# Optimization experiments

Hardware: AMD Instinct MI355X
Metric: run time of the kernel (lower is better)

Reference implementation:

```python
import jax, jax.numpy as jnp
import numpy as np

N_USER, N_ITEM, D = 100000, 50000, 64
H, S, B, L, SUPP, E, HID = 4, 500, 1024, 50, 10000, 1500000, 64

def setup_inputs() -> dict:
    key = jax.random.key(0)
    ks = jax.random.split(key, 24)
    f = lambda k, shp: (jax.random.normal(k, shp, jnp.float32) * 0.1)
    inp = {
        'x': jax.random.randint(ks[0], (B, 2), 0, 50000),
        'history': jax.random.randint(ks[1], (B, L), 0, N_ITEM),
        'history_len': jax.random.randint(ks[2], (B,), 1, L + 1),
        'sample_index': jax.random.randint(ks[3], (H, B, S), 0, SUPP),
        'supp_users': jax.random.randint(ks[4], (SUPP,), 0, N_USER),
        'edge_index': jax.random.randint(ks[5], (2, E), 0, 50000),
        'user_embedding': f(ks[6], (N_USER, D)),
        'item_embedding': f(ks[7], (N_ITEM, D)),
        'wq': f(ks[8], (H, D, D)),
        'wk': f(ks[9], (H, D, D)),
        'wv': f(ks[10], (H, D, D)),
        'w_out_w': f(ks[11], (H * D, D)),
        'gcn_user_w': f(ks[12], (D, D)), 'gcn_user_b': jnp.full((D,), 0.1, jnp.float32),
        'gcn_item_w': f(ks[13], (D, D)), 'gcn_item_b': jnp.full((D,), 0.1, jnp.float32),
        'l1_w': f(ks[14], (4 * D, 2 * HID)), 'l1_b': jnp.full((2 * HID,), 0.1, jnp.float32),
        'l2_w': f(ks[15], (2 * HID, HID)), 'l2_b': jnp.full((HID,), 0.1, jnp.float32),
        'l3_w': f(ks[16], (HID, 1)), 'l3_b': jnp.full((1,), 0.1, jnp.float32),
        'user_bias': jnp.zeros((N_USER, 1), jnp.float32),
        'item_bias': jnp.zeros((N_ITEM, 1), jnp.float32),
    }
    return inp


def _forward(x, history, history_len, sample_index, supp_users, edge_index,
             user_embedding, item_embedding, wq, wk, wv, w_out_w,
             gcn_user_w, gcn_user_b, gcn_item_w, gcn_item_b,
             l1_w, l1_b, l2_w, l2_b, l3_w, l3_b, user_bias, item_bias):
    user_id = x[:, 0]
    item_id = x[:, 1]
    # user init embedding: mean of history item embeddings (original sums unmasked, divides by len)
    user_init_emb = jnp.sum(item_embedding[history], axis=1) / history_len[:, None].astype(jnp.float32)  # [B,D]

    # multi-head RelationGAT over randomly sampled support users
    samp_emb = user_embedding[supp_users[sample_index]]            # [H,B,S,D]
    q = jnp.einsum('bd,hde->hbe', user_init_emb, wq)               # [H,B,D]
    k = jnp.einsum('hbsd,hde->hbse', samp_emb, wk)                 # [H,B,S,D]
    attn = jax.nn.softmax(jnp.einsum('hbe,hbse->hbs', q, k), axis=-1)
    ctx = jnp.einsum('hbs,hbse->hbe', attn, k)                     # [H,B,D]
    gat = jnp.einsum('hbe,hef->hbf', ctx, wv)                      # [H,B,D]
    gat = jnp.transpose(gat, (1, 0, 2)).reshape(gat.shape[1], -1)  # [B,H*D]
    user_emb = gat @ w_out_w                                       # [B,D]

    item_emb = item_embedding[item_id]

    # sparse GCN aggregation via segment_sum (eval mode: no edge dropout)
    eu, ei = edge_index[0], edge_index[1]
    ones_e = jnp.ones((eu.shape[0],), jnp.float32)
    agg_item = jax.ops.segment_sum(item_embedding[ei], eu, num_segments=N_USER)[user_id]
    agg_user = jax.ops.segment_sum(user_embedding[eu], ei, num_segments=N_ITEM)[item_id]
    deg_u = jax.ops.segment_sum(ones_e, eu, num_segments=N_USER)[user_id][:, None] + 1.0
    deg_i = jax.ops.segment_sum(ones_e, ei, num_segments=N_ITEM)[item_id][:, None] + 1.0
    gcn_item_h = agg_item / deg_u
    gcn_user_h = agg_user / deg_i
    gcn_user_out = jax.nn.relu(gcn_user_h @ gcn_user_w + gcn_user_b)
    gcn_item_out = jax.nn.relu(gcn_item_h @ gcn_item_w + gcn_item_b)

    feats = jnp.concatenate([user_emb * item_emb,
                             user_emb * gcn_item_out,
                             gcn_user_out * item_emb,
                             gcn_user_out * gcn_item_out], axis=-1)  # [B,4D]
    h1 = jnp.tanh(feats @ l1_w + l1_b)
    h2 = jnp.tanh(h1 @ l2_w + l2_b)
    score = (h2 @ l3_w + l3_b).reshape(-1)
    return score + user_bias[user_id].reshape(-1) + item_bias[item_id].reshape(-1)


def reference(x, history, history_len, sample_index, supp_users, edge_index,
              user_embedding, item_embedding, wq, wk, wv, w_out_w,
              gcn_user_w, gcn_user_b, gcn_item_w, gcn_item_b,
              l1_w, l1_b, l2_w, l2_b, l3_w, l3_b, user_bias, item_bias):
    return _forward(x, history, history_len, sample_index, supp_users, edge_index,
                    user_embedding, item_embedding, wq, wk, wv, w_out_w,
                    gcn_user_w, gcn_user_b, gcn_item_w, gcn_item_b,
                    l1_w, l1_b, l2_w, l2_b, l3_w, l3_b, user_bias, item_bias)
```

## Files before the change

kernel.cpp:

```cpp
#include <hip/hip_runtime.h>
#include <hip/hip_bf16.h>
#include <math.h>

#define N_USER 100000
#define N_ITEM 50000
#define D 64
#define H 4
#define S 500
#define B 1024
#define L 50
#define SUPP 10000
#define E_EDGES 1500000
#define HID 64
#define N_ID 50000
#define CAP 256
#define BM_WORDS ((N_ID + 31) / 32)

typedef _Float16 half2v __attribute__((ext_vector_type(2)));

#define SUPP_BLKS 625
#define UINIT_BLKS 256
#define PREP1_BLKS 32
#define PREP2_BLKS 64
#define B_UINIT (SUPP_BLKS)
#define B_PREP1 (B_UINIT + UINIT_BLKS)
#define B_PREP2 (B_PREP1 + PREP1_BLKS)
#define B_REP   (B_PREP2 + PREP2_BLKS)
#define SETUP_BLKS (B_REP + 1)

__device__ __forceinline__ ushort f2h(float f) {
  _Float16 h = (_Float16)f;
  return __builtin_bit_cast(ushort, h);
}

__global__ void k_setup(const int* x, const int* history, const int* history_len,
                        const int* supp_users, const float* user_embedding,
                        const float* item_embedding, const float* wq, const float* wk,
                        const float* wv, const float* w_out_w,
                        ushort* supp_h, float* uinit, float* Mmat, float* Pmat,
                        int* user_rep, int* item_rep, int* uctr, int* ictr,
                        unsigned* ubm, unsigned* ibm) {
  __shared__ float smem[64 * 65];
  int blk = blockIdx.x, tid = threadIdx.x;
  if (blk < B_UINIT) {
    int i = blk * 256 + tid;
    if (i < SUPP * 16) {
      int r = i >> 4, c = i & 15;
      float4 v = *(const float4*)&user_embedding[(long)supp_users[r] * 64 + c * 4];
      ushort4 o = {f2h(v.x), f2h(v.y), f2h(v.z), f2h(v.w)};
      *(ushort4*)&supp_h[r * 64 + c * 4] = o;
    }
  } else if (blk < B_PREP1) {
    int b = (blk - B_UINIT) * 4 + (tid >> 6);
    int lane = tid & 63, g = lane >> 4, sub = lane & 15;
    float4 acc = {0.f, 0.f, 0.f, 0.f};
    for (int l = g; l < L; l += 4) {
      int idx = history[b * L + l];
      float4 r = *(const float4*)&item_embedding[(long)idx * 64 + sub * 4];
      acc.x += r.x; acc.y += r.y; acc.z += r.z; acc.w += r.w;
    }
    acc.x += __shfl_xor(acc.x, 16); acc.y += __shfl_xor(acc.y, 16);
    acc.z += __shfl_xor(acc.z, 16); acc.w += __shfl_xor(acc.w, 16);
    acc.x += __shfl_xor(acc.x, 32); acc.y += __shfl_xor(acc.y, 32);
    acc.z += __shfl_xor(acc.z, 32); acc.w += __shfl_xor(acc.w, 32);
    if (lane < 16) {
      float inv = 1.f / (float)history_len[b];
      float4 o = {acc.x * inv, acc.y * inv, acc.z * inv, acc.w * inv};
      *(float4*)&uinit[b * 64 + lane * 4] = o;
    }
  } else if (blk < B_PREP2) {
    int local = blk - B_PREP1;
    int h = local >> 3, bx = local & 7;
    for (int i = tid; i < 64 * 64; i += 256) {
      int row = i >> 6, e = i & 63;
      smem[row * 65 + e] = wk[((long)h * 64 + row) * 64 + e];
    }
    __syncthreads();
    for (int k = 0; k < 2; k++) {
      int oidx = bx * 512 + k * 256 + tid;
      int dp = oidx >> 6, d = oidx & 63;
      float acc = 0.f;
      const float* wqrow = wq + ((long)h * 64 + dp) * 64;
#pragma unroll
      for (int e = 0; e < 64; e++) acc += wqrow[e] * smem[d * 65 + e];
      Mmat[((long)h * 64 + dp) * 64 + d] = acc;
    }
  } else if (blk < B_REP) {
    int local = blk - B_PREP2;
    int p = tid >> 6, lane = tid & 63;
    int gp = local * 4 + p;
    int h = gp >> 6, row = gp & 63;
    float* T = smem + p * 64;
    float tf = 0.f;
#pragma unroll
    for (int e = 0; e < 64; e++)
      tf += wk[((long)h * 64 + row) * 64 + e] * wv[((long)h * 64 + e) * 64 + lane];
    T[lane] = tf;
    __syncthreads();
    float acc = 0.f;
#pragma unroll
    for (int f = 0; f < 64; f++)
      acc += T[f] * w_out_w[((long)h * 64 + f) * 64 + lane];
    Pmat[((long)h * 64 + row) * 64 + lane] = acc;
  } else {
    for (int i = tid; i < BM_WORDS; i += 256) { ubm[i] = 0u; ibm[i] = 0u; }
    __syncthreads();
    for (int gi = tid; gi < B; gi += 256) {
      int u = x[2 * gi], it = x[2 * gi + 1];
      user_rep[u] = gi;
      item_rep[it] = gi;
      atomicOr(&ubm[u >> 5], 1u << (u & 31));
      atomicOr(&ibm[it >> 5], 1u << (it & 31));
      uctr[gi] = 0;
      ictr[gi] = 0;
    }
  }
}

template <int CTRL>
__device__ __forceinline__ float dpp_add(float v) {
  int t = __builtin_amdgcn_update_dpp(0, __float_as_int(v), CTRL, 0xF, 0xF, true);
  return v + __int_as_float(t);
}
#define DPP_XOR1  0xB1
#define DPP_XOR2  0x4E
#define DPP_HMIR  0x141

__device__ __forceinline__ float dot8h(uint4 rv, half2v k0, half2v k1, half2v k2, half2v k3) {
#if __has_builtin(__builtin_amdgcn_fdot2)
  float d = __builtin_amdgcn_fdot2(__builtin_bit_cast(half2v, rv.x), k0, 0.f, false);
  d = __builtin_amdgcn_fdot2(__builtin_bit_cast(half2v, rv.y), k1, d, false);
  d = __builtin_amdgcn_fdot2(__builtin_bit_cast(half2v, rv.z), k2, d, false);
  d = __builtin_amdgcn_fdot2(__builtin_bit_cast(half2v, rv.w), k3, d, false);
  return d;
#else
  half2v a = __builtin_bit_cast(half2v, rv.x), b = __builtin_bit_cast(half2v, rv.y);
  half2v c = __builtin_bit_cast(half2v, rv.z), e = __builtin_bit_cast(half2v, rv.w);
  return (float)a[0] * (float)k0[0] + (float)a[1] * (float)k0[1] +
         (float)b[0] * (float)k1[0] + (float)b[1] * (float)k1[1] +
         (float)c[0] * (float)k2[0] + (float)c[1] * (float)k2[1] +
         (float)e[0] * (float)k3[0] + (float)e[1] * (float)k3[1];
#endif
}

__device__ __forceinline__ void edge_probe(int u, int it,
                                           const int* user_rep, const int* item_rep,
                                           const unsigned* ubm, const unsigned* ibm,
                                           int* uctr, int* ubin, int* ictr, int* ibin) {
  if ((ubm[u >> 5] >> (u & 31)) & 1u) {
    int ru = user_rep[u];
    int pos = atomicAdd(&uctr[ru], 1);
    if (pos < CAP) ubin[ru * CAP + pos] = it;
  }
  if ((ibm[it >> 5] >> (it & 31)) & 1u) {
    int ri = item_rep[it];
    int pos = atomicAdd(&ictr[ri], 1);
    if (pos < CAP) ibin[ri * CAP + pos] = u;
  }
}

__global__ void k_edge(const int* eu, const int* ei,
                       const int* user_rep, const int* item_rep,
                       const unsigned* ubm, const unsigned* ibm,
                       int* uctr, int* ubin, int* ictr, int* ibin) {
  int i = blockIdx.x * 256 + threadIdx.x;
  if (i >= E_EDGES / 2) return;
  int2 u2 = ((const int2*)eu)[i];
  int2 v2 = ((const int2*)ei)[i];
  edge_probe(u2.x, v2.x, user_rep, item_rep, ubm, ibm, uctr, ubin, ictr, ibin);
  edge_probe(u2.y, v2.y, user_rep, item_rep, ubm, ibm, uctr, ubin, ictr, ibin);
}

__global__ void k_attn(const float* uinit, const ushort* supp_h, const int* sample_index,
                       const float* Mmat, const float* Pmat, float* uem4) {
  int tid = threadIdx.x;
  int id = blockIdx.x;
  int h = id >> 10, b = id & 1023;
  int w = tid >> 6, lane = tid & 63;
  int g8 = lane >> 3, sub8 = lane & 7;
  __shared__ float sm_u[64], sm_kq[64], sm_p[256], sm_part[256], sm_den[4];
  __shared__ int sm_sidx[512];

  const int* sidx = sample_index + ((long)h * B + b) * S;
  for (int i = tid; i < 512; i += 256) sm_sidx[i] = (i < S) ? sidx[i] : 0;
  if (tid < 64) sm_u[tid] = uinit[b * 64 + tid];
  __syncthreads();

  const float* Mh = Mmat + h * 64 * 64;
  {
    float p = 0.f;
#pragma unroll
    for (int j = 0; j < 16; j++) p += sm_u[w * 16 + j] * Mh[(w * 16 + j) * 64 + lane];
    sm_p[tid] = p;
  }
  __syncthreads();
  if (tid < 64) sm_kq[tid] = sm_p[tid] + sm_p[64 + tid] + sm_p[128 + tid] + sm_p[192 + tid];
  __syncthreads();

  float4 kqa = *(float4*)&sm_kq[sub8 * 8];
  float4 kqb = *(float4*)&sm_kq[sub8 * 8 + 4];
  half2v k0 = {(_Float16)kqa.x, (_Float16)kqa.y};
  half2v k1 = {(_Float16)kqa.z, (_Float16)kqa.w};
  half2v k2 = {(_Float16)kqb.x, (_Float16)kqb.y};
  half2v k3 = {(_Float16)kqb.z, (_Float16)kqb.w};

  float acc[8] = {0.f, 0.f, 0.f, 0.f, 0.f, 0.f, 0.f, 0.f};
  float den = 0.f;
#pragma unroll 4
  for (int it = 0; it < 16; it++) {
    int s = it * 32 + w * 8 + g8;
    int idx = sm_sidx[s];
    uint4 rv = *(const uint4*)&supp_h[idx * 64 + sub8 * 8];
    float dot = dot8h(rv, k0, k1, k2, k3);
    dot = dpp_add<DPP_XOR1>(dot);
    dot = dpp_add<DPP_XOR2>(dot);
    dot = dpp_add<DPP_HMIR>(dot);
    float e = (s < S) ? __expf(dot) : 0.f;
    den += e;
    half2v r0 = __builtin_bit_cast(half2v, rv.x);
    half2v r1 = __builtin_bit_cast(half2v, rv.y);
    half2v r2 = __builtin_bit_cast(half2v, rv.z);
    half2v r3 = __builtin_bit_cast(half2v, rv.w);
    acc[0] += e * (float)r0[0]; acc[1] += e * (float)r0[1];
    acc[2] += e * (float)r1[0]; acc[3] += e * (float)r1[1];
    acc[4] += e * (float)r2[0]; acc[5] += e * (float)r2[1];
    acc[6] += e * (float)r3[0]; acc[7] += e * (float)r3[1];
  }
#pragma unroll
  for (int j = 0; j < 8; j++) {
    acc[j] += __shfl_xor(acc[j], 8);
    acc[j] += __shfl_xor(acc[j], 16);
    acc[j] += __shfl_xor(acc[j], 32);
  }
  den += __shfl_xor(den, 8); den += __shfl_xor(den, 16); den += __shfl_xor(den, 32);
  if (lane < 8) {
    float4 lo = {acc[0], acc[1], acc[2], acc[3]};
    float4 hi = {acc[4], acc[5], acc[6], acc[7]};
    *(float4*)&sm_part[w * 64 + lane * 8] = lo;
    *(float4*)&sm_part[w * 64 + lane * 8 + 4] = hi;
    if (lane == 0) sm_den[w] = den;
  }
  __syncthreads();
  if (tid < 64) {
    float ws_ = sm_part[tid] + sm_part[64 + tid] + sm_part[128 + tid] + sm_part[192 + tid];
    float dn = sm_den[0] + sm_den[1] + sm_den[2] + sm_den[3];
    sm_u[tid] = ws_ / dn;
  }
  __syncthreads();
  const float* Ph = Pmat + h * 64 * 64;
  {
    float p = 0.f;
#pragma unroll
    for (int j = 0; j < 16; j++) p += sm_u[w * 16 + j] * Ph[(w * 16 + j) * 64 + lane];
    sm_p[tid] = p;
  }
  __syncthreads();
  if (tid < 64)
    uem4[((long)h * B + b) * 64 + tid] =
        sm_p[tid] + sm_p[64 + tid] + sm_p[128 + tid] + sm_p[192 + tid];
}

__global__ void k_final(const int* x, const float* uem4,
                        const float* user_embedding, const float* item_embedding,
                        const int* user_rep, const int* item_rep,
                        const int* uctr, const int* ubin, const int* ictr, const int* ibin,
                        const float* gcn_user_w, const float* gcn_user_b,
                        const float* gcn_item_w, const float* gcn_item_b,
                        const float* l1_w, const float* l1_b,
                        const float* l2_w, const float* l2_b,
                        const float* l3_w, const float* l3_b,
                        const float* user_bias, const float* item_bias, float* out) {
  int b = blockIdx.x, tid = threadIdx.x;
  int side = tid >> 6, lane = tid & 63;
  __shared__ float ue[D], ie[D], agg[2][D], degs[2], guo[D], gio[D],
      feats[4 * D], h1[2 * HID], h2[HID];
  int uid = x[2 * b], iid = x[2 * b + 1];

  {
    int rep = side == 0 ? user_rep[uid] : item_rep[iid];
    int cnt = min((side == 0 ? uctr : ictr)[rep], CAP);
    const int* bin = ((side == 0 ? ubin : ibin)) + rep * CAP;
    const float* emb = side == 0 ? item_embedding : user_embedding;
    float s0 = 0.f, s1 = 0.f, s2 = 0.f, s3 = 0.f;
    int m = 0;
    for (; m + 3 < cnt; m += 4) {
      s0 += emb[(long)bin[m] * 64 + lane];
      s1 += emb[(long)bin[m + 1] * 64 + lane];
      s2 += emb[(long)bin[m + 2] * 64 + lane];
      s3 += emb[(long)bin[m + 3] * 64 + lane];
    }
    for (; m < cnt; m++) s0 += emb[(long)bin[m] * 64 + lane];
    agg[side][lane] = (s0 + s1) + (s2 + s3);
    if (lane == 0) degs[side] = (float)cnt;
  }
  if (tid < D) {
    ue[tid] = uem4[(0L * B + b) * D + tid] + uem4[(1L * B + b) * D + tid] +
              uem4[(2L * B + b) * D + tid] + uem4[(3L * B + b) * D + tid];
    ie[tid] = item_embedding[(long)iid * D + tid];
  }
  __syncthreads();
  if (tid < D) {
    float gih = agg[0][tid] / (degs[0] + 1.f);
    float guh = agg[1][tid] / (degs[1] + 1.f);
    agg[0][tid] = gih;
    agg[1][tid] = guh;
  }
  __syncthreads();
  if (tid < D) {
    float a = 0.f, c = 0.f;
    for (int d = 0; d < D; d++) {
      a += agg[1][d] * gcn_user_w[d * D + tid];
      c += agg[0][d] * gcn_item_w[d * D + tid];
    }
    guo[tid] = fmaxf(a + gcn_user_b[tid], 0.f);
    gio[tid] = fmaxf(c + gcn_item_b[tid], 0.f);
  }
  __syncthreads();
  if (tid < D) {
    feats[tid]         = ue[tid] * ie[tid];
    feats[D + tid]     = ue[tid] * gio[tid];
    feats[2 * D + tid] = guo[tid] * ie[tid];
    feats[3 * D + tid] = guo[tid] * gio[tid];
  }
  __syncthreads();
  {
    float a = 0.f;
    for (int i = 0; i < 4 * D; i++) a += feats[i] * l1_w[i * (2 * HID) + tid];
    h1[tid] = tanhf(a + l1_b[tid]);
  }
  __syncthreads();
  if (tid < HID) {
    float a = 0.f;
    for (int i = 0; i < 2 * HID; i++) a += h1[i] * l2_w[i * HID + tid];
    h2[tid] = tanhf(a + l2_b[tid]);
  }
  __syncthreads();
  if (tid < 64) {
    float v = h2[tid] * l3_w[tid];
#pragma unroll
    for (int off = 32; off > 0; off >>= 1) v += __shfl_xor(v, off);
    if (tid == 0)
      out[b] = v + l3_b[0] + user_bias[uid] + item_bias[iid];
  }
}

extern "C" void kernel_launch(void* const* d_in, const int* in_sizes, int n_in,
                              void* d_out, int out_size, void* d_ws, size_t ws_size,
                              hipStream_t stream) {
  const int* x             = (const int*)d_in[0];
  const int* history       = (const int*)d_in[1];
  const int* history_len   = (const int*)d_in[2];
  const int* sample_index  = (const int*)d_in[3];
  const int* supp_users    = (const int*)d_in[4];
  const int* edge_index    = (const int*)d_in[5];
  const float* user_embedding = (const float*)d_in[6];
  const float* item_embedding = (const float*)d_in[7];
  const float* wq       = (const float*)d_in[8];
  const float* wk       = (const float*)d_in[9];
  const float* wv       = (const float*)d_in[10];
  const float* w_out_w  = (const float*)d_in[11];
  const float* gcn_user_w = (const float*)d_in[12];
  const float* gcn_user_b = (const float*)d_in[13];
  const float* gcn_item_w = (const float*)d_in[14];
  const float* gcn_item_b = (const float*)d_in[15];
  const float* l1_w = (const float*)d_in[16];
  const float* l1_b = (const float*)d_in[17];
  const float* l2_w = (const float*)d_in[18];
  const float* l2_b = (const float*)d_in[19];
  const float* l3_w = (const float*)d_in[20];
  const float* l3_b = (const float*)d_in[21];
  const float* user_bias = (const float*)d_in[22];
  const float* item_bias = (const float*)d_in[23];
  float* out = (float*)d_out;

  float* fws        = (float*)d_ws;
  float* uinit      = fws;
  ushort* supp_h    = (ushort*)(uinit + B * D);
  float* uem4       = uinit + B * D + SUPP * D / 2;
  float* Mmat       = uem4 + (long)H * B * D;
  float* Pmat       = Mmat + H * D * D;
  int* user_rep     = (int*)(Pmat + H * D * D);
  int* item_rep     = user_rep + N_ID;
  int* uctr         = item_rep + N_ID;
  int* ictr         = uctr + B;
  unsigned* ubm     = (unsigned*)(ictr + B);
  unsigned* ibm     = ubm + BM_WORDS;
  int* ubin         = (int*)(ibm + BM_WORDS);
  int* ibin         = ubin + B * CAP;

  const int* eu = edge_index;
  const int* ei = edge_index + E_EDGES;

  k_setup<<<SETUP_BLKS, 256, 0, stream>>>(x, history, history_len, supp_users,
                                          user_embedding, item_embedding, wq, wk, wv,
                                          w_out_w, supp_h, uinit, Mmat, Pmat,
                                          user_rep, item_rep, uctr, ictr, ubm, ibm);
  k_edge<<<(E_EDGES / 2 + 255) / 256, 256, 0, stream>>>(eu, ei, user_rep, item_rep,
                                                        ubm, ibm, uctr, ubin, ictr, ibin);
  k_attn<<<B * H, 256, 0, stream>>>(uinit, supp_h, sample_index, Mmat, Pmat, uem4);
  k_final<<<B, 128, 0, stream>>>(x, uem4, user_embedding, item_embedding,
                                 user_rep, item_rep, uctr, ubin, ictr, ibin,
                                 gcn_user_w, gcn_user_b, gcn_item_w, gcn_item_b,
                                 l1_w, l1_b, l2_w, l2_b, l3_w, l3_b,
                                 user_bias, item_bias, out);
}
```

Baseline: 75.44 us.

## Fuse attention and final MLP into one kernel, one wave per head

Merges the per-(head,batch) attention kernel and the per-batch final MLP/GCN kernel into a single kernel with one block per batch row, where each of four waves handles one head over all 500 samples. This removes a kernel launch and the uem4 intermediate round-trip through global memory. The GCN aggregation is split across four waves, and the l1 matvec across 256 threads. The cost is 4x fewer blocks (1024), each doing a longer serial loop per wave, which may reduce latency hiding on the gather-heavy attention loop. The per-wave sm_kq and sm_wsum reads happen without a barrier between the writing and reading lanes, relying on intra-wave ordering.

```diff
diff --git a/kernel.cpp b/kernel.cpp
--- a/kernel.cpp
+++ b/kernel.cpp
@@ -171,34 +171,43 @@
   edge_probe(u2.y, v2.y, user_rep, item_rep, ubm, ibm, uctr, ubin, ictr, ibin);
 }
 
-__global__ void k_attn(const float* uinit, const ushort* supp_h, const int* sample_index,
-                       const float* Mmat, const float* Pmat, float* uem4) {
-  int tid = threadIdx.x;
-  int id = blockIdx.x;
-  int h = id >> 10, b = id & 1023;
+__global__ __launch_bounds__(256) void k_attnfinal(
+    const int* x, const float* uinit, const ushort* supp_h, const int* sample_index,
+    const float* Mmat, const float* Pmat,
+    const float* user_embedding, const float* item_embedding,
+    const int* user_rep, const int* item_rep,
+    const int* uctr, const int* ubin, const int* ictr, const int* ibin,
+    const float* gcn_user_w, const float* gcn_user_b,
+    const float* gcn_item_w, const float* gcn_item_b,
+    const float* l1_w, const float* l1_b,
+    const float* l2_w, const float* l2_b,
+    const float* l3_w, const float* l3_b,
+    const float* user_bias, const float* item_bias, float* out) {
+  int b = blockIdx.x, tid = threadIdx.x;
   int w = tid >> 6, lane = tid & 63;
   int g8 = lane >> 3, sub8 = lane & 7;
-  __shared__ float sm_u[64], sm_kq[64], sm_p[256], sm_part[256], sm_den[4];
-  __shared__ int sm_sidx[512];
-
-  const int* sidx = sample_index + ((long)h * B + b) * S;
-  for (int i = tid; i < 512; i += 256) sm_sidx[i] = (i < S) ? sidx[i] : 0;
+  __shared__ int sm_sidx[4][512];
+  __shared__ float sm_u[64], sm_kq[4][64], sm_wsum[4][64], sm_p[256];
+  __shared__ float ue[64], ie[64], agg[2][2][64], degs[2], guo[64], gio[64],
+      feats[256], h1[2 * HID], h2[HID];
+
+  int uid = x[2 * b], iid = x[2 * b + 1];
+
+  const int* sidx = sample_index + ((long)w * B + b) * S;
+  for (int i = lane; i < 512; i += 64) sm_sidx[w][i] = (i < S) ? sidx[i] : 0;
   if (tid < 64) sm_u[tid] = uinit[b * 64 + tid];
-  __syncthreads();
-
-  const float* Mh = Mmat + h * 64 * 64;
-  {
-    float p = 0.f;
-#pragma unroll
-    for (int j = 0; j < 16; j++) p += sm_u[w * 16 + j] * Mh[(w * 16 + j) * 64 + lane];
-    sm_p[tid] = p;
-  }
-  __syncthreads();
-  if (tid < 64) sm_kq[tid] = sm_p[tid] + sm_p[64 + tid] + sm_p[128 + tid] + sm_p[192 + tid];
-  __syncthreads();
-
-  float4 kqa = *(float4*)&sm_kq[sub8 * 8];
-  float4 kqb = *(float4*)&sm_kq[sub8 * 8 + 4];
+  if (w == 1) ie[lane] = item_embedding[(long)iid * 64 + lane];
+  __syncthreads();
+
+  const float* Mh = Mmat + w * 4096;
+  {
+    float a = 0.f;
+#pragma unroll
+    for (int d = 0; d < 64; d++) a += sm_u[d] * Mh[d * 64 + lane];
+    sm_kq[w][lane] = a;
+  }
+  float4 kqa = *(float4*)&sm_kq[w][sub8 * 8];
+  float4 kqb = *(float4*)&sm_kq[w][sub8 * 8 + 4];
   half2v k0 = {(_Float16)kqa.x, (_Float16)kqa.y};
   half2v k1 = {(_Float16)kqa.z, (_Float16)kqa.w};
   half2v k2 = {(_Float16)kqb.x, (_Float16)kqb.y};
@@ -207,10 +216,10 @@
   float acc[8] = {0.f, 0.f, 0.f, 0.f, 0.f, 0.f, 0.f, 0.f};
   float den = 0.f;
 #pragma unroll 4
-  for (int it = 0; it < 16; it++) {
-    int s = it * 32 + w * 8 + g8;
-    int idx = sm_sidx[s];
-    uint4 rv = *(const uint4*)&supp_h[idx * 64 + sub8 * 8];
+  for (int it = 0; it < 63; it++) {
+    int s = it * 8 + g8;
+    int idx = sm_sidx[w][s];
+    uint4 rv = *(const uint4*)&supp_h[(long)idx * 64 + sub8 * 8];
     float dot = dot8h(rv, k0, k1, k2, k3);
     dot = dpp_add<DPP_XOR1>(dot);
     dot = dpp_add<DPP_XOR2>(dot);
@@ -233,105 +242,74 @@
     acc[j] += __shfl_xor(acc[j], 32);
   }
   den += __shfl_xor(den, 8); den += __shfl_xor(den, 16); den += __shfl_xor(den, 32);
-  if (lane < 8) {
-    float4 lo = {acc[0], acc[1], acc[2], acc[3]};
-    float4 hi = {acc[4], acc[5], acc[6], acc[7]};
-    *(float4*)&sm_part[w * 64 + lane * 8] = lo;
-    *(float4*)&sm_part[w * 64 + lane * 8 + 4] = hi;
-    if (lane == 0) sm_den[w] = den;
-  }
-  __syncthreads();
-  if (tid < 64) {
-    float ws_ = sm_part[tid] + sm_part[64 + tid] + sm_part[128 + tid] + sm_part[192 + tid];
-    float dn = sm_den[0] + sm_den[1] + sm_den[2] + sm_den[3];
-    sm_u[tid] = ws_ / dn;
-  }
-  __syncthreads();
-  const float* Ph = Pmat + h * 64 * 64;
+  {
+    float inv = 1.f / den;
+    if (lane < 8) {
+      float4 lo = {acc[0] * inv, acc[1] * inv, acc[2] * inv, acc[3] * inv};
+      float4 hi = {acc[4] * inv, acc[5] * inv, acc[6] * inv, acc[7] * inv};
+      *(float4*)&sm_wsum[w][lane * 8] = lo;
+      *(float4*)&sm_wsum[w][lane * 8 + 4] = hi;
+    }
+  }
+
   {
     float p = 0.f;
-#pragma unroll
-    for (int j = 0; j < 16; j++) p += sm_u[w * 16 + j] * Ph[(w * 16 + j) * 64 + lane];
+    const float* Ph = Pmat + w * 4096;
+#pragma unroll
+    for (int d = 0; d < 64; d++) p += sm_wsum[w][d] * Ph[d * 64 + lane];
     sm_p[tid] = p;
   }
-  __syncthreads();
-  if (tid < 64)
-    uem4[((long)h * B + b) * 64 + tid] =
-        sm_p[tid] + sm_p[64 + tid] + sm_p[128 + tid] + sm_p[192 + tid];
-}
-
-__global__ void k_final(const int* x, const float* uem4,
-                        const float* user_embedding, const float* item_embedding,
-                        const int* user_rep, const int* item_rep,
-                        const int* uctr, const int* ubin, const int* ictr, const int* ibin,
-                        const float* gcn_user_w, const float* gcn_user_b,
-                        const float* gcn_item_w, const float* gcn_item_b,
-                        const float* l1_w, const float* l1_b,
-                        const float* l2_w, const float* l2_b,
-                        const float* l3_w, const float* l3_b,
-                        const float* user_bias, const float* item_bias, float* out) {
-  int b = blockIdx.x, tid = threadIdx.x;
-  int side = tid >> 6, lane = tid & 63;
-  __shared__ float ue[D], ie[D], agg[2][D], degs[2], guo[D], gio[D],
-      feats[4 * D], h1[2 * HID], h2[HID];
-  int uid = x[2 * b], iid = x[2 * b + 1];
-
-  {
+
+  {
+    int side = w & 1, part = w >> 1;
     int rep = side == 0 ? user_rep[uid] : item_rep[iid];
     int cnt = min((side == 0 ? uctr : ictr)[rep], CAP);
-    const int* bin = ((side == 0 ? ubin : ibin)) + rep * CAP;
+    const int* bin = (side == 0 ? ubin : ibin) + rep * CAP;
     const float* emb = side == 0 ? item_embedding : user_embedding;
-    float s0 = 0.f, s1 = 0.f, s2 = 0.f, s3 = 0.f;
-    int m = 0;
-    for (; m + 3 < cnt; m += 4) {
+    float s0 = 0.f, s1 = 0.f;
+    int m = part;
+    for (; m + 2 < cnt; m += 4) {
       s0 += emb[(long)bin[m] * 64 + lane];
-      s1 += emb[(long)bin[m + 1] * 64 + lane];
-      s2 += emb[(long)bin[m + 2] * 64 + lane];
-      s3 += emb[(long)bin[m + 3] * 64 + lane];
-    }
-    for (; m < cnt; m++) s0 += emb[(long)bin[m] * 64 + lane];
-    agg[side][lane] = (s0 + s1) + (s2 + s3);
-    if (lane == 0) degs[side] = (float)cnt;
-  }
-  if (tid < D) {
-    ue[tid] = uem4[(0L * B + b) * D + tid] + uem4[(1L * B + b) * D + tid] +
-              uem4[(2L * B + b) * D + tid] + uem4[(3L * B + b) * D + tid];
-    ie[tid] = item_embedding[(long)iid * D + tid];
-  }
-  __syncthreads();
-  if (tid < D) {
-    float gih = agg[0][tid] / (degs[0] + 1.f);
-    float guh = agg[1][tid] / (degs[1] + 1.f);
-    agg[0][tid] = gih;
-    agg[1][tid] = guh;
-  }
-  __syncthreads();
-  if (tid < D) {
+      s1 += emb[(long)bin[m + 2] * 64 + lane];
+    }
+    for (; m < cnt; m += 2) s0 += emb[(long)bin[m] * 64 + lane];
+    agg[side][part][lane] = s0 + s1;
+    if (lane == 0 && part == 0) degs[side] = (float)cnt;
+  }
+  __syncthreads();
+
+  if (tid < 64) {
+    ue[tid] = sm_p[tid] + sm_p[64 + tid] + sm_p[128 + tid] + sm_p[192 + tid];
     float a = 0.f, c = 0.f;
-    for (int d = 0; d < D; d++) {
-      a += agg[1][d] * gcn_user_w[d * D + tid];
-      c += agg[0][d] * gcn_item_w[d * D + tid];
-    }
-    guo[tid] = fmaxf(a + gcn_user_b[tid], 0.f);
-    gio[tid] = fmaxf(c + gcn_item_b[tid], 0.f);
-  }
-  __syncthreads();
-  if (tid < D) {
-    feats[tid]         = ue[tid] * ie[tid];
-    feats[D + tid]     = ue[tid] * gio[tid];
-    feats[2 * D + tid] = guo[tid] * ie[tid];
-    feats[3 * D + tid] = guo[tid] * gio[tid];
-  }
-  __syncthreads();
-  {
+#pragma unroll
+    for (int d = 0; d < 64; d++) {
+      a += (agg[1][0][d] + agg[1][1][d]) * gcn_user_w[d * 64 + tid];
+      c += (agg[0][0][d] + agg[0][1][d]) * gcn_item_w[d * 64 + tid];
+    }
+    guo[tid] = fmaxf(a / (degs[1] + 1.f) + gcn_user_b[tid], 0.f);
+    gio[tid] = fmaxf(c / (degs[0] + 1.f) + gcn_item_b[tid], 0.f);
+  }
+  __syncthreads();
+  if (tid < 64) {
+    feats[tid]        = ue[tid] * ie[tid];
+    feats[64 + tid]   = ue[tid] * gio[tid];
+    feats[128 + tid]  = guo[tid] * ie[tid];
+    feats[192 + tid]  = guo[tid] * gio[tid];
+  }
+  __syncthreads();
+  {
+    int p2 = tid >> 7, o = tid & 127;
     float a = 0.f;
-    for (int i = 0; i < 4 * D; i++) a += feats[i] * l1_w[i * (2 * HID) + tid];
-    h1[tid] = tanhf(a + l1_b[tid]);
-  }
-  __syncthreads();
-  if (tid < HID) {
+    for (int i = p2 * 128; i < p2 * 128 + 128; i++) a += feats[i] * l1_w[i * 128 + o];
+    sm_p[tid] = a;
+  }
+  __syncthreads();
+  if (tid < 128) h1[tid] = tanhf(sm_p[tid] + sm_p[128 + tid] + l1_b[tid]);
+  __syncthreads();
+  if (tid < 64) {
     float a = 0.f;
-    for (int i = 0; i < 2 * HID; i++) a += h1[i] * l2_w[i * HID + tid];
+#pragma unroll
+    for (int i = 0; i < 128; i++) a += h1[i] * l2_w[i * 64 + tid];
     h2[tid] = tanhf(a + l2_b[tid]);
   }
   __syncthreads();
@@ -376,8 +354,7 @@
   float* fws        = (float*)d_ws;
   float* uinit      = fws;
   ushort* supp_h    = (ushort*)(uinit + B * D);
-  float* uem4       = uinit + B * D + SUPP * D / 2;
-  float* Mmat       = uem4 + (long)H * B * D;
+  float* Mmat       = uinit + B * D + SUPP * D / 2;
   float* Pmat       = Mmat + H * D * D;
   int* user_rep     = (int*)(Pmat + H * D * D);
   int* item_rep     = user_rep + N_ID;
@@ -397,10 +374,10 @@
                                           user_rep, item_rep, uctr, ictr, ubm, ibm);
   k_edge<<<(E_EDGES / 2 + 255) / 256, 256, 0, stream>>>(eu, ei, user_rep, item_rep,
                                                         ubm, ibm, uctr, ubin, ictr, ibin);
-  k_attn<<<B * H, 256, 0, stream>>>(uinit, supp_h, sample_index, Mmat, Pmat, uem4);
-  k_final<<<B, 128, 0, stream>>>(x, uem4, user_embedding, item_embedding,
-                                 user_rep, item_rep, uctr, ubin, ictr, ibin,
-                                 gcn_user_w, gcn_user_b, gcn_item_w, gcn_item_b,
-                                 l1_w, l1_b, l2_w, l2_b, l3_w, l3_b,
-                                 user_bias, item_bias, out);
-}
+  k_attnfinal<<<B, 256, 0, stream>>>(x, uinit, supp_h, sample_index, Mmat, Pmat,
+                                     user_embedding, item_embedding,
+                                     user_rep, item_rep, uctr, ubin, ictr, ibin,
+                                     gcn_user_w, gcn_user_b, gcn_item_w, gcn_item_b,
+                                     l1_w, l1_b, l2_w, l2_b, l3_w, l3_b,
+                                     user_bias, item_bias, out);
+}
```

New measurement: 221.7 us. +193.9%, slower.

## Co-schedule setup work with edge binning in one interleaved kernel

Applied to the files above, without the earlier changes.

Moves the user/item representative-table initialisation into its own single-block kernel. The remaining setup work (support-embedding fp16 conversion, history mean, projection-matrix precompute) is then merged with the edge-probing pass into one launch. Blocks are interleaved three edge blocks to one setup block, so the gather-heavy setup work overlaps with the atomic-heavy edge scan instead of running as a separate stage before it. In exchange, edge blocks now carry the setup kernel's shared-memory allocation, which may lower their occupancy, and a tiny serial kernel now sits at the front of the chain.

```diff
diff --git a/kernel.cpp b/kernel.cpp
--- a/kernel.cpp
+++ b/kernel.cpp
@@ -25,30 +25,79 @@
 #define B_UINIT (SUPP_BLKS)
 #define B_PREP1 (B_UINIT + UINIT_BLKS)
 #define B_PREP2 (B_PREP1 + PREP1_BLKS)
-#define B_REP   (B_PREP2 + PREP2_BLKS)
-#define SETUP_BLKS (B_REP + 1)
+#define SETUP_ONLY (B_PREP2 + PREP2_BLKS)
+#define EDGE_BLKS ((E_EDGES / 2 + 255) / 256)
+#define MIX_BLKS (SETUP_ONLY + EDGE_BLKS)
 
 __device__ __forceinline__ ushort f2h(float f) {
   _Float16 h = (_Float16)f;
   return __builtin_bit_cast(ushort, h);
 }
 
-__global__ void k_setup(const int* x, const int* history, const int* history_len,
-                        const int* supp_users, const float* user_embedding,
-                        const float* item_embedding, const float* wq, const float* wk,
-                        const float* wv, const float* w_out_w,
-                        ushort* supp_h, float* uinit, float* Mmat, float* Pmat,
-                        int* user_rep, int* item_rep, int* uctr, int* ictr,
-                        unsigned* ubm, unsigned* ibm) {
+__global__ void k_rep(const int* x, int* user_rep, int* item_rep,
+                      int* uctr, int* ictr, unsigned* ubm, unsigned* ibm) {
+  int tid = threadIdx.x;
+  for (int i = tid; i < BM_WORDS; i += 256) { ubm[i] = 0u; ibm[i] = 0u; }
+  __syncthreads();
+  for (int gi = tid; gi < B; gi += 256) {
+    int u = x[2 * gi], it = x[2 * gi + 1];
+    user_rep[u] = gi;
+    item_rep[it] = gi;
+    atomicOr(&ubm[u >> 5], 1u << (u & 31));
+    atomicOr(&ibm[it >> 5], 1u << (it & 31));
+    uctr[gi] = 0;
+    ictr[gi] = 0;
+  }
+}
+
+__device__ __forceinline__ void edge_probe(int u, int it,
+                                           const int* user_rep, const int* item_rep,
+                                           const unsigned* ubm, const unsigned* ibm,
+                                           int* uctr, int* ubin, int* ictr, int* ibin) {
+  if ((ubm[u >> 5] >> (u & 31)) & 1u) {
+    int ru = user_rep[u];
+    int pos = atomicAdd(&uctr[ru], 1);
+    if (pos < CAP) ubin[ru * CAP + pos] = it;
+  }
+  if ((ibm[it >> 5] >> (it & 31)) & 1u) {
+    int ri = item_rep[it];
+    int pos = atomicAdd(&ictr[ri], 1);
+    if (pos < CAP) ibin[ri * CAP + pos] = u;
+  }
+}
+
+__global__ void k_mix(const int* x, const int* history, const int* history_len,
+                      const int* supp_users, const float* user_embedding,
+                      const float* item_embedding, const float* wq, const float* wk,
+                      const float* wv, const float* w_out_w,
+                      ushort* supp_h, float* uinit, float* Mmat, float* Pmat,
+                      const int* eu, const int* ei,
+                      const int* user_rep, const int* item_rep,
+                      const unsigned* ubm, const unsigned* ibm,
+                      int* uctr, int* ubin, int* ictr, int* ibin) {
   __shared__ float smem[64 * 65];
-  int blk = blockIdx.x, tid = threadIdx.x;
+  int tid = threadIdx.x;
+  int sq = blockIdx.x >> 2, r = blockIdx.x & 3;
+
+  if (r != 3) {
+    int edge_id = 3 * sq + r;
+    int i = edge_id * 256 + tid;
+    if (i >= E_EDGES / 2) return;
+    int2 u2 = ((const int2*)eu)[i];
+    int2 v2 = ((const int2*)ei)[i];
+    edge_probe(u2.x, v2.x, user_rep, item_rep, ubm, ibm, uctr, ubin, ictr, ibin);
+    edge_probe(u2.y, v2.y, user_rep, item_rep, ubm, ibm, uctr, ubin, ictr, ibin);
+    return;
+  }
+
+  int blk = sq;
   if (blk < B_UINIT) {
     int i = blk * 256 + tid;
     if (i < SUPP * 16) {
-      int r = i >> 4, c = i & 15;
-      float4 v = *(const float4*)&user_embedding[(long)supp_users[r] * 64 + c * 4];
+      int rr = i >> 4, c = i & 15;
+      float4 v = *(const float4*)&user_embedding[(long)supp_users[rr] * 64 + c * 4];
       ushort4 o = {f2h(v.x), f2h(v.y), f2h(v.z), f2h(v.w)};
-      *(ushort4*)&supp_h[r * 64 + c * 4] = o;
+      *(ushort4*)&supp_h[rr * 64 + c * 4] = o;
     }
   } else if (blk < B_PREP1) {
     int b = (blk - B_UINIT) * 4 + (tid >> 6);
@@ -56,8 +105,8 @@
     float4 acc = {0.f, 0.f, 0.f, 0.f};
     for (int l = g; l < L; l += 4) {
       int idx = history[b * L + l];
-      float4 r = *(const float4*)&item_embedding[(long)idx * 64 + sub * 4];
-      acc.x += r.x; acc.y += r.y; acc.z += r.z; acc.w += r.w;
+      float4 rv = *(const float4*)&item_embedding[(long)idx * 64 + sub * 4];
+      acc.x += rv.x; acc.y += rv.y; acc.z += rv.z; acc.w += rv.w;
     }
     acc.x += __shfl_xor(acc.x, 16); acc.y += __shfl_xor(acc.y, 16);
     acc.z += __shfl_xor(acc.z, 16); acc.w += __shfl_xor(acc.w, 16);
@@ -85,7 +134,7 @@
       for (int e = 0; e < 64; e++) acc += wqrow[e] * smem[d * 65 + e];
       Mmat[((long)h * 64 + dp) * 64 + d] = acc;
     }
-  } else if (blk < B_REP) {
+  } else {
     int local = blk - B_PREP2;
     int p = tid >> 6, lane = tid & 63;
     int gp = local * 4 + p;
@@ -102,18 +151,6 @@
     for (int f = 0; f < 64; f++)
       acc += T[f] * w_out_w[((long)h * 64 + f) * 64 + lane];
     Pmat[((long)h * 64 + row) * 64 + lane] = acc;
-  } else {
-    for (int i = tid; i < BM_WORDS; i += 256) { ubm[i] = 0u; ibm[i] = 0u; }
-    __syncthreads();
-    for (int gi = tid; gi < B; gi += 256) {
-      int u = x[2 * gi], it = x[2 * gi + 1];
-      user_rep[u] = gi;
-      item_rep[it] = gi;
-      atomicOr(&ubm[u >> 5], 1u << (u & 31));
-      atomicOr(&ibm[it >> 5], 1u << (it & 31));
-      uctr[gi] = 0;
-      ictr[gi] = 0;
-    }
   }
 }
 
@@ -141,34 +178,6 @@
          (float)c[0] * (float)k2[0] + (float)c[1] * (float)k2[1] +
          (float)e[0] * (float)k3[0] + (float)e[1] * (float)k3[1];
 #endif
-}
-
-__device__ __forceinline__ void edge_probe(int u, int it,
-                                           const int* user_rep, const int* item_rep,
-                                           const unsigned* ubm, const unsigned* ibm,
-                                           int* uctr, int* ubin, int* ictr, int* ibin) {
-  if ((ubm[u >> 5] >> (u & 31)) & 1u) {
-    int ru = user_rep[u];
-    int pos = atomicAdd(&uctr[ru], 1);
-    if (pos < CAP) ubin[ru * CAP + pos] = it;
-  }
-  if ((ibm[it >> 5] >> (it & 31)) & 1u) {
-    int ri = item_rep[it];
-    int pos = atomicAdd(&ictr[ri], 1);
-    if (pos < CAP) ibin[ri * CAP + pos] = u;
-  }
-}
-
-__global__ void k_edge(const int* eu, const int* ei,
-                       const int* user_rep, const int* item_rep,
-                       const unsigned* ubm, const unsigned* ibm,
-                       int* uctr, int* ubin, int* ictr, int* ibin) {
-  int i = blockIdx.x * 256 + threadIdx.x;
-  if (i >= E_EDGES / 2) return;
-  int2 u2 = ((const int2*)eu)[i];
-  int2 v2 = ((const int2*)ei)[i];
-  edge_probe(u2.x, v2.x, user_rep, item_rep, ubm, ibm, uctr, ubin, ictr, ibin);
-  edge_probe(u2.y, v2.y, user_rep, item_rep, ubm, ibm, uctr, ubin, ictr, ibin);
 }
 
 __global__ void k_attn(const float* uinit, const ushort* supp_h, const int* sample_index,
@@ -391,12 +400,12 @@
   const int* eu = edge_index;
   const int* ei = edge_index + E_EDGES;
 
-  k_setup<<<SETUP_BLKS, 256, 0, stream>>>(x, history, history_len, supp_users,
-                                          user_embedding, item_embedding, wq, wk, wv,
-                                          w_out_w, supp_h, uinit, Mmat, Pmat,
-                                          user_rep, item_rep, uctr, ictr, ubm, ibm);
-  k_edge<<<(E_EDGES / 2 + 255) / 256, 256, 0, stream>>>(eu, ei, user_rep, item_rep,
-                                                        ubm, ibm, uctr, ubin, ictr, ibin);
+  k_rep<<<1, 256, 0, stream>>>(x, user_rep, item_rep, uctr, ictr, ubm, ibm);
+  k_mix<<<MIX_BLKS, 256, 0, stream>>>(x, history, history_len, supp_users,
+                                      user_embedding, item_embedding, wq, wk, wv,
+                                      w_out_w, supp_h, uinit, Mmat, Pmat,
+                                      eu, ei, user_rep, item_rep, ubm, ibm,
+                                      uctr, ubin, ictr, ibin);
   k_attn<<<B * H, 256, 0, stream>>>(uinit, supp_h, sample_index, Mmat, Pmat, uem4);
   k_final<<<B, 128, 0, stream>>>(x, uem4, user_embedding, item_embedding,
                                  user_rep, item_rep, uctr, ubin, ictr, ibin,
```

Measured after the change: 78.61 us. +4.2%, slower.
